# Kernel optimization log

Hardware: AMD Instinct MI355X
Metric: run time of the kernel (lower is better)

The kernel has to match this reference:

```python
import jax, jax.numpy as jnp
import numpy as np

CONV_DIMS = (-3, -2)   # spatial dims (channel-last layout)
RADIUS = (3, 3)        # window = 1 + 2*r = 7 per dim -> 49 cells
STEP = (1, 1)


def _unfold(x, dim, window, step):
    """torch.Tensor.unfold: dim -> out_len, window appended as last axis."""
    dim = dim % x.ndim
    n = x.shape[dim]
    starts = jnp.arange((n - window) // step + 1) * step          # [L]
    idx = starts[:, None] + jnp.arange(window)[None, :]           # [L, w]
    y = jnp.take(x, idx, axis=dim)                                # dim -> [L, w]
    return jnp.moveaxis(y, dim + 1, -1)                           # window axis to last


def _local_attention(x):
    # Unfold each conv dim; move its window axis to the front (as in the torch code).
    for i, r, s in zip(CONV_DIMS, RADIUS, STEP):
        x = _unfold(x, i, 1 + 2 * r, s)
        x = jnp.moveaxis(x, -1, 0)
    n_win = len(CONV_DIMS)
    cells = int(np.prod(x.shape[:n_win]))
    x = x.reshape((cells,) + x.shape[n_win:])      # [cells, B, H', W', C]
    center = cells // 2                            # spatial center of the window
    q = jnp.moveaxis(x[center:center + 1], 0, -2)  # [B, H', W', 1, C]
    k = jnp.moveaxis(jnp.concatenate([x[:center], x[center + 1:]], axis=0), 0, -2)  # [B,H',W',cells-1,C]
    d = q.shape[-1]
    scores = jnp.einsum('...qc,...kc->...qk', q, k) / jnp.sqrt(jnp.asarray(d, q.dtype))
    w = jax.nn.softmax(scores, axis=-1)
    out = jnp.einsum('...qk,...kc->...qc', w, k)   # keys double as values
    return out.squeeze(-2)                          # [B, H', W', C]


def setup_inputs() -> dict:
    key = jax.random.key(0)
    X = jax.random.normal(key, (4, 64, 64, 256), dtype=jnp.float32)
    return {"X": X}


def reference(X):
    return _local_attention(X)
```

## Files before the change

### kernel.cpp

```cpp
#include <hip/hip_runtime.h>

#define B_   4
#define H_   64
#define W_   64
#define C_   256
#define HO_  58
#define WO_  58
#define JP   29
#define GRID (B_ * HO_ * JP)
#define PERX (GRID / 8)

typedef __attribute__((ext_vector_type(4))) float f32x4;
typedef __attribute__((ext_vector_type(2))) float f32x2;

template <int CTRL>
__device__ __forceinline__ float dpp_add(float p) {
    int t = __builtin_amdgcn_update_dpp(0, __builtin_bit_cast(int, p),
                                        CTRL, 0xF, 0xF, true);
    return p + __builtin_bit_cast(float, t);
}
__device__ __forceinline__ float reduce32_dpp(float p) {
    p = dpp_add<0x111>(p);
    p = dpp_add<0x112>(p);
    p = dpp_add<0x114>(p);
    p = dpp_add<0x118>(p);
    p = dpp_add<0x142>(p);
    return p;
}

__global__ __launch_bounds__(256, 4) void convnd_attn_kernel(const float* __restrict__ X,
                                                             float* __restrict__ out) {
    __shared__ __align__(8)  float sAB[64][2];
    __shared__ __align__(16) float pacc0[8 * C_];
    __shared__ __align__(16) float pacc1[8 * C_];

    const int sp  = (blockIdx.x & 7) * PERX + (blockIdx.x >> 3);
    const int jp  = sp % JP;
    const int t1  = sp / JP;
    const int i   = t1 % HO_;
    const int b   = t1 / HO_;
    const int j0  = jp * 2;

    const int tid  = threadIdx.x;
    const int wave = tid >> 6;
    const int lane = tid & 63;
    const int g    = lane >> 5;
    const int sub  = lane & 31;

    const float* base = X + (size_t)b * H_ * W_ * C_;
    const int co = 8 * sub;

    const float* qp0 = base + ((i + 3) * W_ + (j0 + 3)) * C_ + co;
    const f32x4 scale = {0.0625f, 0.0625f, 0.0625f, 0.0625f};
    const f32x4 qa0 = *(const f32x4*)(qp0)       * scale;
    const f32x4 qa1 = *(const f32x4*)(qp0 + 4)   * scale;
    const f32x4 qb0 = *(const f32x4*)(qp0 + C_)  * scale;
    const f32x4 qb1 = *(const f32x4*)(qp0 + C_ + 4) * scale;

    f32x4 kv[7][2];
    const int cell0 = wave * 14 + g;
    #pragma unroll
    for (int r = 0; r < 7; ++r) {
        const int cell = cell0 + 2 * r;
        const int di = cell >> 3, dj = cell & 7;
        const float* kp = base + ((i + di) * W_ + (j0 + dj)) * C_ + co;
        kv[r][0] = *(const f32x4*)(kp);
        kv[r][1] = *(const f32x4*)(kp + 4);
    }

    #pragma unroll
    for (int r = 0; r < 7; ++r) {
        f32x4 d0 = kv[r][0] * qa0;
        d0 = __builtin_elementwise_fma(kv[r][1], qa1, d0);
        f32x4 d1 = kv[r][0] * qb0;
        d1 = __builtin_elementwise_fma(kv[r][1], qb1, d1);
        f32x2 h0 = __builtin_shufflevector(d0, d0, 0, 1) + __builtin_shufflevector(d0, d0, 2, 3);
        f32x2 h1 = __builtin_shufflevector(d1, d1, 0, 1) + __builtin_shufflevector(d1, d1, 2, 3);
        float p0 = h0.x + h0.y;
        float p1 = h1.x + h1.y;
        p0 = reduce32_dpp(p0);
        p1 = reduce32_dpp(p1);
        if (sub == 31) {
            const int cell = cell0 + 2 * r;
            f32x2 pp = {p0, p1};
            *(f32x2*)&sAB[cell][0] = pp;
        }
    }
    __syncthreads();

    if (wave == 0) {
        const int dj = lane & 7;
        const bool valid = (lane < 56) && (dj <= 6) && (lane != 27);
        const float e = valid ? __expf(sAB[lane & 63][0]) : 0.f;
        float t = e;
        #pragma unroll
        for (int m = 32; m; m >>= 1) t += __shfl_xor(t, m, 64);
        if (lane < 56) sAB[lane][0] = e / t;
    } else if (wave == 1) {
        const int dj = lane & 7;
        const bool valid = (lane < 56) && (dj >= 1) && (lane != 28);
        const float e = valid ? __expf(sAB[lane & 63][1]) : 0.f;
        float t = e;
        #pragma unroll
        for (int m = 32; m; m >>= 1) t += __shfl_xor(t, m, 64);
        if (lane < 56) sAB[lane][1] = e / t;
    }
    __syncthreads();

    f32x4 a00 = {0,0,0,0}, a01 = {0,0,0,0};
    f32x4 a10 = {0,0,0,0}, a11 = {0,0,0,0};
    #pragma unroll
    for (int r = 0; r < 7; ++r) {
        const int cell = cell0 + 2 * r;
        const f32x2 w2 = *(const f32x2*)&sAB[cell][0];
        const f32x4 w0s = {w2.x, w2.x, w2.x, w2.x};
        const f32x4 w1s = {w2.y, w2.y, w2.y, w2.y};
        a00 = __builtin_elementwise_fma(w0s, kv[r][0], a00);
        a01 = __builtin_elementwise_fma(w0s, kv[r][1], a01);
        a10 = __builtin_elementwise_fma(w1s, kv[r][0], a10);
        a11 = __builtin_elementwise_fma(w1s, kv[r][1], a11);
    }
    {
        const int row = (wave * 2 + g) * C_ + co;
        *(f32x4*)&pacc0[row]     = a00;
        *(f32x4*)&pacc0[row + 4] = a01;
        *(f32x4*)&pacc1[row]     = a10;
        *(f32x4*)&pacc1[row + 4] = a11;
    }
    __syncthreads();

    float s0 = 0.f, s1 = 0.f;
    #pragma unroll
    for (int p = 0; p < 8; ++p) {
        s0 += pacc0[p * C_ + tid];
        s1 += pacc1[p * C_ + tid];
    }
    float* o = out + ((size_t)(b * HO_ + i) * WO_ + j0) * C_ + tid;
    o[0]  = s0;
    o[C_] = s1;
}

extern "C" void kernel_launch(void* const* d_in, const int* in_sizes, int n_in,
                              void* d_out, int out_size, void* d_ws, size_t ws_size,
                              hipStream_t stream) {
    const float* X = (const float*)d_in[0];
    float* outp    = (float*)d_out;
    hipLaunchKernelGGL(convnd_attn_kernel,
                       dim3(GRID), dim3(256), 0, stream, X, outp);
}
```

Before: 85.66 us.

## Tile output as 2x2 pixel blocks to share loaded key windows

Each block now computes a 2x2 tile of output pixels from one shared 8x8 key window instead of a 1x2 pair from a 7x8 window. This cuts the number of blocks in half and raises reuse of each loaded key vector from 2 to 4 queries, lowering global load traffic per output. In exchange it uses more registers (four query and four accumulator sets), doubles shared memory for partial sums, and adds padding blocks that exit early.

```diff
diff --git a/kernel.cpp b/kernel.cpp
--- a/kernel.cpp
+++ b/kernel.cpp
@@ -6,9 +6,9 @@
 #define C_   256
 #define HO_  58
 #define WO_  58
-#define JP   29
-#define GRID (B_ * HO_ * JP)
-#define PERX (GRID / 8)
+#define TPB  841
+#define NT   3364
+#define GRID 3368
 
 typedef __attribute__((ext_vector_type(4))) float f32x4;
 typedef __attribute__((ext_vector_type(2))) float f32x2;
@@ -30,114 +30,111 @@
 
 __global__ __launch_bounds__(256, 4) void convnd_attn_kernel(const float* __restrict__ X,
                                                              float* __restrict__ out) {
-    __shared__ __align__(8)  float sAB[64][2];
-    __shared__ __align__(16) float pacc0[8 * C_];
-    __shared__ __align__(16) float pacc1[8 * C_];
+    __shared__ __align__(16) float sAB[64][4];
+    __shared__ __align__(16) float pacc[4][8][C_];
 
-    const int sp  = (blockIdx.x & 7) * PERX + (blockIdx.x >> 3);
-    const int jp  = sp % JP;
-    const int t1  = sp / JP;
-    const int i   = t1 % HO_;
-    const int b   = t1 / HO_;
-    const int j0  = jp * 2;
+    const int sp = (blockIdx.x & 7) * 421 + (blockIdx.x >> 3);
+    if (sp >= NT) return;
+    const int b   = sp / TPB;
+    const int rem = sp - b * TPB;
+    const int ti  = rem / 29;
+    const int tj  = rem - ti * 29;
+    const int i0  = 2 * ti;
+    const int j0  = 2 * tj;
 
     const int tid  = threadIdx.x;
     const int wave = tid >> 6;
     const int lane = tid & 63;
     const int g    = lane >> 5;
     const int sub  = lane & 31;
+    const int co   = 8 * sub;
 
     const float* base = X + (size_t)b * H_ * W_ * C_;
-    const int co = 8 * sub;
 
-    const float* qp0 = base + ((i + 3) * W_ + (j0 + 3)) * C_ + co;
     const f32x4 scale = {0.0625f, 0.0625f, 0.0625f, 0.0625f};
-    const f32x4 qa0 = *(const f32x4*)(qp0)       * scale;
-    const f32x4 qa1 = *(const f32x4*)(qp0 + 4)   * scale;
-    const f32x4 qb0 = *(const f32x4*)(qp0 + C_)  * scale;
-    const f32x4 qb1 = *(const f32x4*)(qp0 + C_ + 4) * scale;
+    f32x4 q[4][2];
+    #pragma unroll
+    for (int px = 0; px < 4; ++px) {
+        const int pi = px >> 1, pj = px & 1;
+        const float* qp = base + ((i0 + 3 + pi) * W_ + (j0 + 3 + pj)) * C_ + co;
+        q[px][0] = *(const f32x4*)(qp)     * scale;
+        q[px][1] = *(const f32x4*)(qp + 4) * scale;
+    }
 
-    f32x4 kv[7][2];
-    const int cell0 = wave * 14 + g;
+    f32x4 kv[8][2];
+    const int cell0 = wave * 16 + g;
     #pragma unroll
-    for (int r = 0; r < 7; ++r) {
+    for (int r = 0; r < 8; ++r) {
         const int cell = cell0 + 2 * r;
-        const int di = cell >> 3, dj = cell & 7;
-        const float* kp = base + ((i + di) * W_ + (j0 + dj)) * C_ + co;
+        const int ci = cell >> 3, cj = cell & 7;
+        const float* kp = base + ((i0 + ci) * W_ + (j0 + cj)) * C_ + co;
         kv[r][0] = *(const f32x4*)(kp);
         kv[r][1] = *(const f32x4*)(kp + 4);
     }
 
     #pragma unroll
-    for (int r = 0; r < 7; ++r) {
-        f32x4 d0 = kv[r][0] * qa0;
-        d0 = __builtin_elementwise_fma(kv[r][1], qa1, d0);
-        f32x4 d1 = kv[r][0] * qb0;
-        d1 = __builtin_elementwise_fma(kv[r][1], qb1, d1);
-        f32x2 h0 = __builtin_shufflevector(d0, d0, 0, 1) + __builtin_shufflevector(d0, d0, 2, 3);
-        f32x2 h1 = __builtin_shufflevector(d1, d1, 0, 1) + __builtin_shufflevector(d1, d1, 2, 3);
-        float p0 = h0.x + h0.y;
-        float p1 = h1.x + h1.y;
-        p0 = reduce32_dpp(p0);
-        p1 = reduce32_dpp(p1);
+    for (int r = 0; r < 8; ++r) {
+        float p[4];
+        #pragma unroll
+        for (int px = 0; px < 4; ++px) {
+            f32x4 d = kv[r][0] * q[px][0];
+            d = __builtin_elementwise_fma(kv[r][1], q[px][1], d);
+            f32x2 h = __builtin_shufflevector(d, d, 0, 1) + __builtin_shufflevector(d, d, 2, 3);
+            p[px] = reduce32_dpp(h.x + h.y);
+        }
         if (sub == 31) {
             const int cell = cell0 + 2 * r;
-            f32x2 pp = {p0, p1};
-            *(f32x2*)&sAB[cell][0] = pp;
+            f32x4 pk = {p[0], p[1], p[2], p[3]};
+            *(f32x4*)&sAB[cell][0] = pk;
         }
     }
     __syncthreads();
 
-    if (wave == 0) {
-        const int dj = lane & 7;
-        const bool valid = (lane < 56) && (dj <= 6) && (lane != 27);
-        const float e = valid ? __expf(sAB[lane & 63][0]) : 0.f;
+    {
+        const int pi = wave >> 1, pj = wave & 1;
+        const int ci = lane >> 3, cj = lane & 7;
+        const bool valid = (ci >= pi) && (ci <= pi + 6) && (cj >= pj) && (cj <= pj + 6)
+                           && !(ci == pi + 3 && cj == pj + 3);
+        const float e = valid ? __expf(sAB[lane][wave]) : 0.f;
         float t = e;
         #pragma unroll
         for (int m = 32; m; m >>= 1) t += __shfl_xor(t, m, 64);
-        if (lane < 56) sAB[lane][0] = e / t;
-    } else if (wave == 1) {
-        const int dj = lane & 7;
-        const bool valid = (lane < 56) && (dj >= 1) && (lane != 28);
-        const float e = valid ? __expf(sAB[lane & 63][1]) : 0.f;
-        float t = e;
-        #pragma unroll
-        for (int m = 32; m; m >>= 1) t += __shfl_xor(t, m, 64);
-        if (lane < 56) sAB[lane][1] = e / t;
+        sAB[lane][wave] = e / t;
     }
     __syncthreads();
 
-    f32x4 a00 = {0,0,0,0}, a01 = {0,0,0,0};
-    f32x4 a10 = {0,0,0,0}, a11 = {0,0,0,0};
+    f32x4 a[4][2];
     #pragma unroll
-    for (int r = 0; r < 7; ++r) {
+    for (int px = 0; px < 4; ++px) { a[px][0] = (f32x4){0,0,0,0}; a[px][1] = (f32x4){0,0,0,0}; }
+    #pragma unroll
+    for (int r = 0; r < 8; ++r) {
         const int cell = cell0 + 2 * r;
-        const f32x2 w2 = *(const f32x2*)&sAB[cell][0];
-        const f32x4 w0s = {w2.x, w2.x, w2.x, w2.x};
-        const f32x4 w1s = {w2.y, w2.y, w2.y, w2.y};
-        a00 = __builtin_elementwise_fma(w0s, kv[r][0], a00);
-        a01 = __builtin_elementwise_fma(w0s, kv[r][1], a01);
-        a10 = __builtin_elementwise_fma(w1s, kv[r][0], a10);
-        a11 = __builtin_elementwise_fma(w1s, kv[r][1], a11);
+        const f32x4 w4 = *(const f32x4*)&sAB[cell][0];
+        #pragma unroll
+        for (int px = 0; px < 4; ++px) {
+            const f32x4 ws = {w4[px], w4[px], w4[px], w4[px]};
+            a[px][0] = __builtin_elementwise_fma(ws, kv[r][0], a[px][0]);
+            a[px][1] = __builtin_elementwise_fma(ws, kv[r][1], a[px][1]);
+        }
     }
     {
-        const int row = (wave * 2 + g) * C_ + co;
-        *(f32x4*)&pacc0[row]     = a00;
-        *(f32x4*)&pacc0[row + 4] = a01;
-        *(f32x4*)&pacc1[row]     = a10;
-        *(f32x4*)&pacc1[row + 4] = a11;
+        const int row = wave * 2 + g;
+        #pragma unroll
+        for (int px = 0; px < 4; ++px) {
+            *(f32x4*)&pacc[px][row][co]     = a[px][0];
+            *(f32x4*)&pacc[px][row][co + 4] = a[px][1];
+        }
     }
     __syncthreads();
 
-    float s0 = 0.f, s1 = 0.f;
     #pragma unroll
-    for (int p = 0; p < 8; ++p) {
-        s0 += pacc0[p * C_ + tid];
-        s1 += pacc1[p * C_ + tid];
+    for (int px = 0; px < 4; ++px) {
+        const int pi = px >> 1, pj = px & 1;
+        float s = 0.f;
+        #pragma unroll
+        for (int rr = 0; rr < 8; ++rr) s += pacc[px][rr][tid];
+        out[((size_t)(b * HO_ + i0 + pi) * WO_ + (j0 + pj)) * C_ + tid] = s;
     }
-    float* o = out + ((size_t)(b * HO_ + i) * WO_ + j0) * C_ + tid;
-    o[0]  = s0;
-    o[C_] = s1;
 }
 
 extern "C" void kernel_launch(void* const* d_in, const int* in_sizes, int n_in,
```

Result: no change. 87.36 us (+2.0%).
